# Performance work log

Hardware: AMD Instinct MI355X
Metric: run time of the kernel (lower is better)

Reference implementation:

```python
import jax, jax.numpy as jnp
import numpy as np

WINDOW = 11
CHANNEL = 3
SIGMA = 1.5


def _gaussian_kernel():
    coords = jnp.arange(WINDOW, dtype=jnp.float32) - (WINDOW - 1) / 2.0
    g = jnp.exp(-(coords ** 2) / (2.0 * SIGMA ** 2))
    g = g / g.sum()
    k2d = g[:, None] * g[None, :]                      # (k, k)
    # depthwise kernel, OIHW with feature_group_count=C -> (C, 1, k, k)
    return jnp.tile(k2d[None, None], (CHANNEL, 1, 1, 1))


def _dwconv(x, kernel):
    pad = WINDOW // 2
    return jax.lax.conv_general_dilated(
        x, kernel, window_strides=(1, 1),
        padding=((pad, pad), (pad, pad)),
        dimension_numbers=("NCHW", "OIHW", "NCHW"),
        feature_group_count=CHANNEL)


def setup_inputs() -> dict:
    key = jax.random.key(0)
    k1, k2 = jax.random.split(key)
    B, C, H, W = 32, 3, 512, 512
    denoised = jax.random.uniform(k1, (B, C, H, W), dtype=jnp.float32)
    clean = jax.random.uniform(k2, (B, C, H, W), dtype=jnp.float32)
    return {"denoised": denoised, "clean": clean}


def reference(denoised, clean):
    kernel = _gaussian_kernel()
    img1 = jnp.clip(denoised, 0.0, 1.0)
    img2 = jnp.clip(clean, 0.0, 1.0)

    mu1 = _dwconv(img1, kernel)
    mu2 = _dwconv(img2, kernel)
    mu1_sq = mu1 * mu1
    mu2_sq = mu2 * mu2
    mu1_mu2 = mu1 * mu2
    sigma1_sq = _dwconv(img1 * img1, kernel) - mu1_sq
    sigma2_sq = _dwconv(img2 * img2, kernel) - mu2_sq
    sigma12 = _dwconv(img1 * img2, kernel) - mu1_mu2

    C1 = 0.01 ** 2
    C2 = 0.03 ** 2
    ssim_map = ((2.0 * mu1_mu2 + C1) * (2.0 * sigma12 + C2)) / (
        (mu1_sq + mu2_sq + C1) * (sigma1_sq + sigma2_sq + C2))
    return 1.0 - ssim_map.mean()
```

## Files before the change

### kernel.cpp

```cpp
#include <hip/hip_runtime.h>

#define IMG 512
#define OUT_R 16
#define OUT_C 64
#define HALO 5
#define NVTILE 5
#define VS 88
#define NT 256
#define NSLOTS 64

typedef _Float16 f16x8 __attribute__((ext_vector_type(8)));
typedef _Float16 h2    __attribute__((ext_vector_type(2)));
typedef float    f32x4 __attribute__((ext_vector_type(4)));

static constexpr float GWf[11] = {
    0.00102838f, 0.00759876f, 0.03600077f, 0.10936053f, 0.21300556f,
    0.26601170f, 0.21300556f, 0.10936053f, 0.03600077f, 0.00759876f,
    0.00102838f };

struct WTab { alignas(16) _Float16 v[4][16][8]; };
static constexpr WTab make_wtab() {
    WTab t{};
    for (int g = 0; g < 4; ++g)
        for (int j = 0; j < 16; ++j)
            for (int b = 0; b < 8; ++b) {
                const int d = 8 * g + b - j;
                t.v[g][j][b] = (d >= 0 && d <= 10) ? (_Float16)GWf[d]
                                                   : (_Float16)0.f;
            }
    return t;
}
__device__ constexpr WTab WT = make_wtab();

struct SMem {
    _Float16 vb[4][OUT_R][VS];
    float red[4];
};

__device__ __forceinline__ h2 cvt_pk(float a, float b) {
#if __has_builtin(__builtin_amdgcn_cvt_pkrtz)
    auto r = __builtin_amdgcn_cvt_pkrtz(a, b);
    union { decltype(r) i; h2 o; } u; u.i = r;
    return u.o;
#else
    h2 r; r[0] = (_Float16)a; r[1] = (_Float16)b; return r;
#endif
}

__device__ __forceinline__ void vert_tile(
    int tl, int c0, int y0, size_t pbase,
    const float* __restrict__ den, const float* __restrict__ cln,
    int fj, int fg, f16x8 wf, SMem* sm)
{
    const int gc = c0 - HALO + tl * 16 + fj;
    const bool colok = (unsigned)gc < IMG;
    const int rbase = y0 - HALO + 8 * fg;

    float xr[8], yr[8];
#pragma unroll
    for (int b = 0; b < 8; ++b) {
        const int gr = rbase + b;
        const bool ok = colok && ((unsigned)gr < IMG) && (8 * fg + b < 26);
        float xv = 0.f, yv = 0.f;
        if (ok) {
            const size_t idx = pbase + (size_t)gr * IMG + gc;
            xv = den[idx]; yv = cln[idx];
        }
        xr[b] = xv; yr[b] = yv;
    }

    union { f16x8 v; h2 p[4]; } fx, fy, fq, fp;
#pragma unroll
    for (int bb = 0; bb < 4; ++bb) {
        const float x0 = fminf(fmaxf(xr[2 * bb], 0.f), 1.f);
        const float x1 = fminf(fmaxf(xr[2 * bb + 1], 0.f), 1.f);
        const float ya = fminf(fmaxf(yr[2 * bb], 0.f), 1.f);
        const float yb = fminf(fmaxf(yr[2 * bb + 1], 0.f), 1.f);
        const h2 xh = cvt_pk(x0, x1);
        const h2 yh = cvt_pk(ya, yb);
        fx.p[bb] = xh;
        fy.p[bb] = yh;
        fq.p[bb] = xh * xh + yh * yh;
        fp.p[bb] = xh * yh;
    }

    const f32x4 zero4 = {0.f, 0.f, 0.f, 0.f};
    const f32x4 a0 = __builtin_amdgcn_mfma_f32_16x16x32_f16(wf, fx.v, zero4, 0, 0, 0);
    const f32x4 a1 = __builtin_amdgcn_mfma_f32_16x16x32_f16(wf, fy.v, zero4, 0, 0, 0);
    const f32x4 a2 = __builtin_amdgcn_mfma_f32_16x16x32_f16(wf, fq.v, zero4, 0, 0, 0);
    const f32x4 a3 = __builtin_amdgcn_mfma_f32_16x16x32_f16(wf, fp.v, zero4, 0, 0, 0);

    const int cc = tl * 16 + fj;
#pragma unroll
    for (int b = 0; b < 4; ++b) {
        const int r = 4 * fg + b;
        sm->vb[0][r][cc] = (_Float16)a0[b];
        sm->vb[1][r][cc] = (_Float16)a1[b];
        sm->vb[2][r][cc] = (_Float16)a2[b];
        sm->vb[3][r][cc] = (_Float16)a3[b];
    }
}

__global__ __launch_bounds__(NT, 6)
void ssim_mfma(const float* __restrict__ den, const float* __restrict__ cln,
               double* __restrict__ slots) {
    __shared__ SMem sm;

    const int t    = threadIdx.x;
    const int lane = t & 63;
    const int w    = t >> 6;
    const int fj   = lane & 15;
    const int fg   = lane >> 4;

    const int bid = blockIdx.x;
    const int chunk = gridDim.x >> 3;
    const int vid = (bid & 7) * chunk + (bid >> 3);

    const int rs    = vid & 31;
    const int cs    = (vid >> 5) & 7;
    const int plane = vid >> 8;
    const int c0 = cs * OUT_C;
    const int y0 = rs * OUT_R;
    const size_t pbase = (size_t)plane * (IMG * IMG);

    const f16x8 wf = *reinterpret_cast<const f16x8*>(WT.v[fg][fj]);
    const f32x4 zero4 = {0.f, 0.f, 0.f, 0.f};

    vert_tile(w, c0, y0, pbase, den, cln, fj, fg, wf, &sm);
    if (w == 0)
        vert_tile(4, c0, y0, pbase, den, cln, fj, fg, wf, &sm);
    __syncthreads();

    float sacc = 0.f;
    {
        f32x4 d[4];
#pragma unroll
        for (int ch = 0; ch < 4; ++ch) {
            const f16x8 af = *reinterpret_cast<const f16x8*>(
                &sm.vb[ch][fj][w * 16 + 8 * fg]);
            d[ch] = __builtin_amdgcn_mfma_f32_16x16x32_f16(af, wf, zero4, 0, 0, 0);
        }
#pragma unroll
        for (int b = 0; b < 4; ++b) {
            const float C1 = 1e-4f, C2 = 9e-4f;
            const float mu1 = d[0][b], mu2 = d[1][b];
            const float qb  = d[2][b], pb  = d[3][b];
            const float mu1s = mu1 * mu1, mu2s = mu2 * mu2, mu12 = mu1 * mu2;
            const float ssum = qb - mu1s - mu2s;
            const float s12  = pb - mu12;
            const float num = fmaf(2.f, mu12, C1) * fmaf(2.f, s12, C2);
            const float dnm = (mu1s + mu2s + C1) * (ssum + C2);
            sacc = fmaf(num, __builtin_amdgcn_rcpf(dnm), sacc);
        }
    }

#pragma unroll
    for (int off = 32; off > 0; off >>= 1)
        sacc += __shfl_down(sacc, off, 64);
    if (lane == 0) sm.red[w] = sacc;
    __syncthreads();
    if (t == 0) {
        const float s = sm.red[0] + sm.red[1] + sm.red[2] + sm.red[3];
        atomicAdd(&slots[(size_t)(bid & (NSLOTS - 1)) * 8], (double)s);
    }
}

__global__ void ssim_finalize(const double* __restrict__ slots,
                              float* __restrict__ out, double inv_n) {
    double s = 0.0;
    for (int i = 0; i < NSLOTS; ++i) s += slots[i * 8];
    out[0] = 1.0f - (float)(s * inv_n);
}

extern "C" void kernel_launch(void* const* d_in, const int* in_sizes, int n_in,
                              void* d_out, int out_size, void* d_ws,
                              size_t ws_size, hipStream_t stream) {
    const float* den = (const float*)d_in[0];
    const float* cln = (const float*)d_in[1];
    float* out = (float*)d_out;
    double* slots = (double*)d_ws;

    (void)hipMemsetAsync(d_ws, 0, NSLOTS * 64, stream);

    const int n = in_sizes[0];
    const int planes = n / (IMG * IMG);
    dim3 grid(planes * (IMG / OUT_R) * (IMG / OUT_C));
    ssim_mfma<<<grid, NT, 0, stream>>>(den, cln, slots);
    ssim_finalize<<<1, 1, 0, stream>>>(slots, out, 1.0 / (double)n);
}
```

Baseline: 306.0 us.

## Process 128-row strips per block with register-prefetched chunk windows

Each block now walks a 128-row strip in 16-row chunks instead of handling one 16-row tile. The input window for the next chunk is loaded into registers while the current chunk's MFMAs and SSIM math run, so global load latency is hidden. The fifth column tile's vertical pass is split across the four waves, one channel each, instead of being done entirely by wave 0, which removes that load imbalance. In exchange there are two extra barriers per chunk, higher register pressure from the double window buffers, and an eight-times smaller grid.

After: 306.7 us. About the same (+0.2%).

```diff
diff --git a/kernel.cpp b/kernel.cpp
--- a/kernel.cpp
+++ b/kernel.cpp
@@ -1,10 +1,11 @@
 #include <hip/hip_runtime.h>
 
 #define IMG 512
-#define OUT_R 16
 #define OUT_C 64
+#define STRIP_R 128
+#define CHUNK 16
+#define NITER (STRIP_R / CHUNK)
 #define HALO 5
-#define NVTILE 5
 #define VS 88
 #define NT 256
 #define NSLOTS 64
@@ -33,7 +34,7 @@
 __device__ constexpr WTab WT = make_wtab();
 
 struct SMem {
-    _Float16 vb[4][OUT_R][VS];
+    _Float16 vb[4][CHUNK][VS];
     float red[4];
 };
 
@@ -47,35 +48,37 @@
 #endif
 }
 
-__device__ __forceinline__ void vert_tile(
-    int tl, int c0, int y0, size_t pbase,
+__device__ __forceinline__ void load_win(
+    int tl, int ytop, int c0, size_t pbase,
     const float* __restrict__ den, const float* __restrict__ cln,
-    int fj, int fg, f16x8 wf, SMem* sm)
+    int fj, int fg, float Px[8], float Py[8])
 {
     const int gc = c0 - HALO + tl * 16 + fj;
     const bool colok = (unsigned)gc < IMG;
-    const int rbase = y0 - HALO + 8 * fg;
-
-    float xr[8], yr[8];
+    const int rbase = ytop - HALO + 8 * fg;
 #pragma unroll
     for (int b = 0; b < 8; ++b) {
         const int gr = rbase + b;
-        const bool ok = colok && ((unsigned)gr < IMG) && (8 * fg + b < 26);
+        const bool ok = colok && ((unsigned)gr < IMG);
         float xv = 0.f, yv = 0.f;
         if (ok) {
             const size_t idx = pbase + (size_t)gr * IMG + gc;
             xv = den[idx]; yv = cln[idx];
         }
-        xr[b] = xv; yr[b] = yv;
-    }
-
-    union { f16x8 v; h2 p[4]; } fx, fy, fq, fp;
+        Px[b] = xv; Py[b] = yv;
+    }
+}
+
+union Frag { f16x8 v; h2 p[4]; };
+
+__device__ __forceinline__ void pack_all(const float Px[8], const float Py[8],
+                                         Frag& fx, Frag& fy, Frag& fq, Frag& fp) {
 #pragma unroll
     for (int bb = 0; bb < 4; ++bb) {
-        const float x0 = fminf(fmaxf(xr[2 * bb], 0.f), 1.f);
-        const float x1 = fminf(fmaxf(xr[2 * bb + 1], 0.f), 1.f);
-        const float ya = fminf(fmaxf(yr[2 * bb], 0.f), 1.f);
-        const float yb = fminf(fmaxf(yr[2 * bb + 1], 0.f), 1.f);
+        const float x0 = fminf(fmaxf(Px[2 * bb], 0.f), 1.f);
+        const float x1 = fminf(fmaxf(Px[2 * bb + 1], 0.f), 1.f);
+        const float ya = fminf(fmaxf(Py[2 * bb], 0.f), 1.f);
+        const float yb = fminf(fmaxf(Py[2 * bb + 1], 0.f), 1.f);
         const h2 xh = cvt_pk(x0, x1);
         const h2 yh = cvt_pk(ya, yb);
         fx.p[bb] = xh;
@@ -83,21 +86,22 @@
         fq.p[bb] = xh * xh + yh * yh;
         fp.p[bb] = xh * yh;
     }
-
-    const f32x4 zero4 = {0.f, 0.f, 0.f, 0.f};
-    const f32x4 a0 = __builtin_amdgcn_mfma_f32_16x16x32_f16(wf, fx.v, zero4, 0, 0, 0);
-    const f32x4 a1 = __builtin_amdgcn_mfma_f32_16x16x32_f16(wf, fy.v, zero4, 0, 0, 0);
-    const f32x4 a2 = __builtin_amdgcn_mfma_f32_16x16x32_f16(wf, fq.v, zero4, 0, 0, 0);
-    const f32x4 a3 = __builtin_amdgcn_mfma_f32_16x16x32_f16(wf, fp.v, zero4, 0, 0, 0);
-
-    const int cc = tl * 16 + fj;
-#pragma unroll
-    for (int b = 0; b < 4; ++b) {
-        const int r = 4 * fg + b;
-        sm->vb[0][r][cc] = (_Float16)a0[b];
-        sm->vb[1][r][cc] = (_Float16)a1[b];
-        sm->vb[2][r][cc] = (_Float16)a2[b];
-        sm->vb[3][r][cc] = (_Float16)a3[b];
+}
+
+__device__ __forceinline__ void pack_ch(const float Px[8], const float Py[8],
+                                        int ch, Frag& f) {
+#pragma unroll
+    for (int bb = 0; bb < 4; ++bb) {
+        const float x0 = fminf(fmaxf(Px[2 * bb], 0.f), 1.f);
+        const float x1 = fminf(fmaxf(Px[2 * bb + 1], 0.f), 1.f);
+        const float ya = fminf(fmaxf(Py[2 * bb], 0.f), 1.f);
+        const float yb = fminf(fmaxf(Py[2 * bb + 1], 0.f), 1.f);
+        const h2 xh = cvt_pk(x0, x1);
+        const h2 yh = cvt_pk(ya, yb);
+        if (ch == 0)      f.p[bb] = xh;
+        else if (ch == 1) f.p[bb] = yh;
+        else if (ch == 2) f.p[bb] = xh * xh + yh * yh;
+        else              f.p[bb] = xh * yh;
     }
 }
 
@@ -116,23 +120,53 @@
     const int chunk = gridDim.x >> 3;
     const int vid = (bid & 7) * chunk + (bid >> 3);
 
-    const int rs    = vid & 31;
-    const int cs    = (vid >> 5) & 7;
-    const int plane = vid >> 8;
+    const int rs    = vid & 3;
+    const int cs    = (vid >> 2) & 7;
+    const int plane = vid >> 5;
     const int c0 = cs * OUT_C;
-    const int y0 = rs * OUT_R;
+    const int y0 = rs * STRIP_R;
     const size_t pbase = (size_t)plane * (IMG * IMG);
 
     const f16x8 wf = *reinterpret_cast<const f16x8*>(WT.v[fg][fj]);
     const f32x4 zero4 = {0.f, 0.f, 0.f, 0.f};
 
-    vert_tile(w, c0, y0, pbase, den, cln, fj, fg, wf, &sm);
-    if (w == 0)
-        vert_tile(4, c0, y0, pbase, den, cln, fj, fg, wf, &sm);
-    __syncthreads();
+    float Px[8], Py[8], P4x[8], P4y[8];
+    load_win(w, y0, c0, pbase, den, cln, fj, fg, Px, Py);
+    load_win(4, y0, c0, pbase, den, cln, fj, fg, P4x, P4y);
 
     float sacc = 0.f;
-    {
+    for (int it = 0; it < NITER; ++it) {
+        const int yo = y0 + CHUNK * it;
+
+        Frag fx, fy, fq, fp, f4;
+        pack_all(Px, Py, fx, fy, fq, fp);
+        pack_ch(P4x, P4y, w, f4);
+
+        if (it < NITER - 1) {
+            load_win(w, yo + CHUNK, c0, pbase, den, cln, fj, fg, Px, Py);
+            load_win(4, yo + CHUNK, c0, pbase, den, cln, fj, fg, P4x, P4y);
+        }
+
+        const f32x4 a0 = __builtin_amdgcn_mfma_f32_16x16x32_f16(wf, fx.v, zero4, 0, 0, 0);
+        const f32x4 a1 = __builtin_amdgcn_mfma_f32_16x16x32_f16(wf, fy.v, zero4, 0, 0, 0);
+        const f32x4 a2 = __builtin_amdgcn_mfma_f32_16x16x32_f16(wf, fq.v, zero4, 0, 0, 0);
+        const f32x4 a3 = __builtin_amdgcn_mfma_f32_16x16x32_f16(wf, fp.v, zero4, 0, 0, 0);
+        const f32x4 a4 = __builtin_amdgcn_mfma_f32_16x16x32_f16(wf, f4.v, zero4, 0, 0, 0);
+
+        __syncthreads();
+
+        const int cc = w * 16 + fj;
+#pragma unroll
+        for (int b = 0; b < 4; ++b) {
+            const int r = 4 * fg + b;
+            sm.vb[0][r][cc] = (_Float16)a0[b];
+            sm.vb[1][r][cc] = (_Float16)a1[b];
+            sm.vb[2][r][cc] = (_Float16)a2[b];
+            sm.vb[3][r][cc] = (_Float16)a3[b];
+            sm.vb[w][r][64 + fj] = (_Float16)a4[b];
+        }
+        __syncthreads();
+
         f32x4 d[4];
 #pragma unroll
         for (int ch = 0; ch < 4; ++ch) {
@@ -184,7 +218,7 @@
 
     const int n = in_sizes[0];
     const int planes = n / (IMG * IMG);
-    dim3 grid(planes * (IMG / OUT_R) * (IMG / OUT_C));
+    dim3 grid(planes * (IMG / STRIP_R) * (IMG / OUT_C));
     ssim_mfma<<<grid, NT, 0, stream>>>(den, cln, slots);
     ssim_finalize<<<1, 1, 0, stream>>>(slots, out, 1.0 / (double)n);
 }
```
